# Kernel optimization log

Measured on AMD Instinct MI355X. Metric: run time of the kernel, lower is better.

The kernel has to match this reference:

```python
import jax, jax.numpy as jnp
import numpy as np
from jax import lax

NGTH = 15  # num_gth_mem
EPS = 1e-5  # BatchNorm eps


def _conv(x, w, b):
    y = lax.conv_general_dilated(x, w, (1, 1), 'VALID',
                                 dimension_numbers=('NCHW', 'OIHW', 'NCHW'))
    return y + b[None, :, None, None]


def _bn(x, g, b, m, v):
    # eval-mode BatchNorm2d with running stats
    return g[None, :, None, None] * (x - m[None, :, None, None]) * lax.rsqrt(v[None, :, None, None] + EPS) + b[None, :, None, None]


def _masked_stats(x, w):
    # x: (B, M, ...) ; w: (B, M) float weights. Population mean/std over masked mem slots.
    extra = (1,) * (x.ndim - 2)
    we = w.reshape(w.shape[:2] + extra)
    cnt = jnp.sum(w, axis=1).reshape((w.shape[0],) + extra)
    s = jnp.sum(x * we, axis=1)
    ss = jnp.sum(x * x * we, axis=1)
    mean = s / cnt
    var = jnp.maximum(ss / cnt - mean * mean, 0.0)
    return mean, jnp.sqrt(var)


def _forward(target_scores, ptm, pmt, predicted_iou, mem_mask, params):
    nf, ns, nmem, c, h, w = ptm.shape
    B = nf * ns
    ts = target_scores.reshape(B, 1, h, w)
    pmt = pmt.reshape(B, nmem, 1, h, w)
    ptm = ptm.reshape(B, nmem, c, h, w)
    mask = mem_mask.reshape(B, nmem)
    piou = predicted_iou.reshape(B, 1, 1, 1)

    mf = mask.astype(ts.dtype)
    # rank of each selected slot within the masked (ordered) selection
    rank = jnp.cumsum(mf, axis=1) - 1.0
    gth_w = mf * (rank < NGTH).astype(ts.dtype)   # first NGTH selected slots
    oth_w = mf * (rank >= NGTH).astype(ts.dtype)  # remaining selected slots

    max_ts = jnp.max(ts.reshape(B, -1), axis=1)

    pmt_mean, pmt_std = _masked_stats(pmt, mf)                 # (B,1,h,w)
    pmt_gth = pmt[:, :NGTH]                                    # unmasked slice (as in torch code)
    pmt_gth_mean = jnp.mean(pmt_gth, axis=1)
    pmt_gth_std = jnp.std(pmt_gth, axis=1)
    pmt_oth_mean, pmt_oth_std = _masked_stats(pmt, oth_w)

    ptm_max = jnp.max(ptm.reshape(B, nmem, -1), axis=2)        # (B, nmem)
    m_mm, s_mm = _masked_stats(ptm_max, mf)
    m_gm, s_gm = _masked_stats(ptm_max, gth_w)
    m_om, s_om = _masked_stats(ptm_max, oth_w)

    def bcast(v):
        return jnp.broadcast_to(v.reshape(B, 1, 1, 1), (B, 1, h, w))

    inp = jnp.concatenate([
        bcast(max_ts), jnp.broadcast_to(piou, (B, 1, h, w)),
        pmt_mean, pmt_std, pmt_gth_mean, pmt_gth_std, pmt_oth_mean, pmt_oth_std,
        bcast(m_mm), bcast(s_mm), bcast(m_gm), bcast(s_gm), bcast(m_om), bcast(s_om)
    ], axis=1)  # (B, 14, h, w)

    (c1w, c1b, g1, b1, m1, v1, c2w, c2b, g2, b2, m2, v2,
     c3w, c3b, g3, b3, m3, v3, c4w, c4b) = params
    x = jax.nn.relu(_bn(_conv(inp, c1w, c1b), g1, b1, m1, v1))
    x = lax.reduce_window(x, -jnp.inf, lax.max, (1, 1, 2, 2), (1, 1, 2, 2), 'VALID')
    x = jax.nn.relu(_bn(_conv(x, c2w, c2b), g2, b2, m2, v2))
    x = jax.nn.relu(_bn(_conv(x, c3w, c3b), g3, b3, m3, v3))
    x = _conv(x, c4w, c4b)
    return jnp.max(x, axis=(2, 3), keepdims=True)  # AdaptiveMaxPool2d((1,1)) -> (B,1,1,1)


def setup_inputs() -> dict:
    key = jax.random.key(0)
    ks = jax.random.split(key, 16)
    nf, ns, nmem, h, w = 16, 32, 30, 32, 32
    d = {}
    d['target_scores'] = jax.random.normal(ks[0], (nf, ns, 1, h, w), jnp.float32)
    d['ptm'] = jax.random.uniform(ks[1], (nf, ns, nmem, 1, h, w), jnp.float32)
    d['pmt'] = jax.random.uniform(ks[2], (nf, ns, nmem, 1, h, w), jnp.float32)
    d['predicted_iou'] = jax.random.uniform(ks[3], (nf, ns), jnp.float32)
    mask = jax.random.uniform(ks[4], (nf, ns, nmem)) < 0.7
    mask = mask.at[..., :20].set(True)  # >= 20 selected -> 'other' set non-empty
    d['mem_mask'] = mask
    d['conv1_w'] = jax.random.normal(ks[5], (64, 14, 3, 3), jnp.float32) * 0.1
    d['conv1_b'] = jnp.zeros((64,), jnp.float32)
    d['bn1_g'] = jnp.ones((64,), jnp.float32); d['bn1_b'] = jnp.zeros((64,), jnp.float32)
    d['bn1_m'] = jnp.zeros((64,), jnp.float32); d['bn1_v'] = jnp.ones((64,), jnp.float32)
    d['conv2_w'] = jax.random.normal(ks[6], (64, 64, 3, 3), jnp.float32) * 0.05
    d['conv2_b'] = jnp.zeros((64,), jnp.float32)
    d['bn2_g'] = jnp.ones((64,), jnp.float32); d['bn2_b'] = jnp.zeros((64,), jnp.float32)
    d['bn2_m'] = jnp.zeros((64,), jnp.float32); d['bn2_v'] = jnp.ones((64,), jnp.float32)
    d['conv3_w'] = jax.random.normal(ks[7], (64, 64, 3, 3), jnp.float32) * 0.05
    d['conv3_b'] = jnp.zeros((64,), jnp.float32)
    d['bn3_g'] = jnp.ones((64,), jnp.float32); d['bn3_b'] = jnp.zeros((64,), jnp.float32)
    d['bn3_m'] = jnp.zeros((64,), jnp.float32); d['bn3_v'] = jnp.ones((64,), jnp.float32)
    d['conv4_w'] = jax.random.normal(ks[8], (1, 64, 3, 3), jnp.float32) * 0.05
    d['conv4_b'] = jnp.zeros((1,), jnp.float32)
    return d


def reference(target_scores, ptm, pmt, predicted_iou, mem_mask,
              conv1_w, conv1_b, bn1_g, bn1_b, bn1_m, bn1_v,
              conv2_w, conv2_b, bn2_g, bn2_b, bn2_m, bn2_v,
              conv3_w, conv3_b, bn3_g, bn3_b, bn3_m, bn3_v,
              conv4_w, conv4_b):
    params = (conv1_w, conv1_b, bn1_g, bn1_b, bn1_m, bn1_v,
              conv2_w, conv2_b, bn2_g, bn2_b, bn2_m, bn2_v,
              conv3_w, conv3_b, bn3_g, bn3_b, bn3_m, bn3_v,
              conv4_w, conv4_b)
    return _forward(target_scores, ptm, pmt, predicted_iou, mem_mask, params)
```

## Files before the change

### kernel.cpp

```cpp
#include <hip/hip_runtime.h>
#include <math.h>

#define NFB  512
#define NMEM 30
#define PIX  1024
#define EPSF 1e-5f

typedef _Float16 half8_t __attribute__((ext_vector_type(8)));
typedef _Float16 half4_t __attribute__((ext_vector_type(4)));
typedef float float4_t __attribute__((ext_vector_type(4)));

#define OFF_W2R   13631488
#define OFF_W3R   13705216
#define OFF_WR1   13778944
#define OFF_WSUM1 13791232

__global__ __launch_bounds__(256) void k_prep(
    const float* __restrict__ c1w, const float* __restrict__ c2w,
    const float* __restrict__ c3w, _Float16* __restrict__ w2rep,
    _Float16* __restrict__ w3rep, _Float16* __restrict__ wr1,
    float* __restrict__ wsum1)
{
  int i = blockIdx.x * 256 + threadIdx.x;
  if (i < 36864) {
    int kr = i / 12288, rem = i - kr * 12288;
    int oc = rem / 192, k = rem - oc * 192;
    int kc = k >> 6, ci = k & 63;
    w2rep[i] = (_Float16)c2w[((oc * 64 + ci) * 3 + kr) * 3 + kc];
  } else if (i < 73728) {
    int j = i - 36864;
    int kr = j / 12288, rem = j - kr * 12288;
    int oc = rem / 192, k = rem - oc * 192;
    int kc = k >> 6, ci = k & 63;
    w3rep[j] = (_Float16)c3w[((oc * 64 + ci) * 3 + kr) * 3 + kc];
  } else if (i < 79872) {
    int j = i - 73728;
    int kr = j / 2048, rem = j - kr * 2048;
    int oc = rem >> 5, k = rem & 31;
    int kc = k >> 3, ci = k & 7;
    _Float16 v = (_Float16)0.f;
    if (kc < 3 && ci < 6)
      v = (_Float16)c1w[((oc * 14 + (2 + ci)) * 3 + kr) * 3 + kc];
    wr1[j] = v;
  } else if (i < 80384) {
    int j = i - 79872;
    int oc = j >> 3, u = j & 7;
    const int uch[8] = {0, 1, 8, 9, 10, 11, 12, 13};
    const float* wp = c1w + (oc * 14 + uch[u]) * 9;
    float s = 0.f;
    #pragma unroll
    for (int k = 0; k < 9; ++k) s += wp[k];
    wsum1[j] = s;
  }
}

__global__ __launch_bounds__(256, 2) void k_mega(
    const float* __restrict__ ts, const float* __restrict__ ptm,
    const float* __restrict__ pmt, const float* __restrict__ piou,
    const int* __restrict__ mask,
    const _Float16* __restrict__ wr1, const float* __restrict__ wsum1,
    const float* __restrict__ c1b, const float* __restrict__ g1,
    const float* __restrict__ b1, const float* __restrict__ m1,
    const float* __restrict__ v1,
    const _Float16* __restrict__ w2rep,
    const float* __restrict__ c2b, const float* __restrict__ g2,
    const float* __restrict__ b2, const float* __restrict__ m2,
    const float* __restrict__ v2,
    const _Float16* __restrict__ w3rep,
    const float* __restrict__ c3b, const float* __restrict__ g3,
    const float* __restrict__ b3, const float* __restrict__ m3,
    const float* __restrict__ v3,
    const float* __restrict__ c4w, const float* __restrict__ c4b,
    float* __restrict__ out)
{
  __shared__ __align__(16) char s_buf[55296];
  __shared__ float s_wm[NMEM], s_wo[NMEM], s_pmax[NMEM];
  __shared__ float s_red[4], s_scal[12], s_cnt[4];
  __shared__ float s_w4[576];

  const int b = blockIdx.x, t = threadIdx.x;
  const int lane = t & 63, wave = t >> 6;
  const int n16 = lane & 15, q = lane >> 4;
  _Float16* const IMG = (_Float16*)s_buf;
  _Float16* const X1  = (_Float16*)(s_buf + 16448);
  _Float16* const X2S = (_Float16*)s_buf;
  _Float16* const X3  = (_Float16*)(s_buf + 29952);

  for (int i = t; i < 576; i += 256) {
    int ci = i / 9, k = i - ci * 9;
    s_w4[k * 64 + ci] = c4w[i];
  }
  if (t == 0) {
    float cum = 0.f, cm = 0.f, cg = 0.f, co = 0.f;
    for (int m = 0; m < NMEM; ++m) {
      float f  = (mask[b * NMEM + m] != 0) ? 1.f : 0.f;
      float gg = (cum < 15.f) ? f : 0.f;
      float oo = f - gg;
      cum += f;
      s_wm[m] = f; s_wo[m] = oo;
      cm += f; cg += gg; co += oo;
    }
    s_cnt[0] = cm; s_cnt[1] = cg; s_cnt[2] = co;
  }
  {
    float4 u[8][4];
    const float* pb = ptm + (size_t)b * NMEM * PIX + lane * 4;
    #pragma unroll
    for (int k = 0; k < 8; ++k) {
      int m = wave + 4 * k;
      if (m < NMEM) {
        const float* p = pb + (size_t)m * PIX;
        #pragma unroll
        for (int j = 0; j < 4; ++j) u[k][j] = *(const float4*)(p + j * 256);
      }
    }
    #pragma unroll
    for (int k = 0; k < 8; ++k) {
      int m = wave + 4 * k;
      if (m < NMEM) {
        float4 v0 = u[k][0], v1_ = u[k][1], v2_ = u[k][2], v3_ = u[k][3];
        float mx = fmaxf(fmaxf(fmaxf(v0.x, v0.y), fmaxf(v0.z, v0.w)),
                         fmaxf(fmaxf(v1_.x, v1_.y), fmaxf(v1_.z, v1_.w)));
        mx = fmaxf(mx, fmaxf(fmaxf(fmaxf(v2_.x, v2_.y), fmaxf(v2_.z, v2_.w)),
                             fmaxf(fmaxf(v3_.x, v3_.y), fmaxf(v3_.z, v3_.w))));
        #pragma unroll
        for (int off = 32; off > 0; off >>= 1)
          mx = fmaxf(mx, __shfl_down(mx, off, 64));
        if (lane == 0) s_pmax[m] = mx;
      }
    }
  }
  {
    float4 v = ((const float4*)(ts + (size_t)b * PIX))[t];
    float mx = fmaxf(fmaxf(v.x, v.y), fmaxf(v.z, v.w));
    #pragma unroll
    for (int off = 32; off > 0; off >>= 1)
      mx = fmaxf(mx, __shfl_down(mx, off, 64));
    if (lane == 0) s_red[wave] = mx;
  }
  __syncthreads();
  if (t == 0) {
    float maxts = fmaxf(fmaxf(s_red[0], s_red[1]), fmaxf(s_red[2], s_red[3]));
    float sm = 0, sm2 = 0, sg = 0, sg2 = 0, so = 0, so2 = 0;
    for (int m = 0; m < NMEM; ++m) {
      float x = s_pmax[m];
      float gg = s_wm[m] - s_wo[m];
      sm += s_wm[m] * x;  sm2 += s_wm[m] * x * x;
      sg += gg * x;       sg2 += gg * x * x;
      so += s_wo[m] * x;  so2 += s_wo[m] * x * x;
    }
    float cm = s_cnt[0], cg = s_cnt[1], co = s_cnt[2];
    float a = sm / cm, g = sg / cg, o = so / co;
    s_scal[0] = maxts; s_scal[1] = piou[b];
    s_scal[2] = a; s_scal[3] = sqrtf(fmaxf(sm2 / cm - a * a, 0.f));
    s_scal[4] = g; s_scal[5] = sqrtf(fmaxf(sg2 / cg - g * g, 0.f));
    s_scal[6] = o; s_scal[7] = sqrtf(fmaxf(so2 / co - o * o, 0.f));
  }
  {
    const float cm = s_cnt[0], co = s_cnt[2];
    const int p0 = t * 4;
    const float* pb = pmt + (size_t)b * NMEM * PIX + p0;
    float4 va[15], vb[15];
    #pragma unroll
    for (int j = 0; j < 15; ++j) va[j] = *(const float4*)(pb + (size_t)j * PIX);
    #pragma unroll
    for (int j = 0; j < 15; ++j) vb[j] = *(const float4*)(pb + (size_t)(15 + j) * PIX);
    float sA[4] = {0,0,0,0}, qA[4] = {0,0,0,0};
    float sG[4] = {0,0,0,0}, qG[4] = {0,0,0,0};
    float sO[4] = {0,0,0,0}, qO[4] = {0,0,0,0};
    #pragma unroll
    for (int j = 0; j < 15; ++j) {
      float wm = s_wm[j], wo = s_wo[j];
      float xv[4] = {va[j].x, va[j].y, va[j].z, va[j].w};
      #pragma unroll
      for (int k = 0; k < 4; ++k) {
        float x = xv[k];
        sA[k] = fmaf(wm, x, sA[k]); qA[k] = fmaf(wm * x, x, qA[k]);
        sO[k] = fmaf(wo, x, sO[k]); qO[k] = fmaf(wo * x, x, qO[k]);
        sG[k] += x; qG[k] = fmaf(x, x, qG[k]);
      }
    }
    #pragma unroll
    for (int j = 0; j < 15; ++j) {
      float wm = s_wm[15 + j], wo = s_wo[15 + j];
      float xv[4] = {vb[j].x, vb[j].y, vb[j].z, vb[j].w};
      #pragma unroll
      for (int k = 0; k < 4; ++k) {
        float x = xv[k];
        sA[k] = fmaf(wm, x, sA[k]); qA[k] = fmaf(wm * x, x, qA[k]);
        sO[k] = fmaf(wo, x, sO[k]); qO[k] = fmaf(wo * x, x, qO[k]);
      }
    }
    half8_t* ob = (half8_t*)(IMG) + p0;
    #pragma unroll
    for (int j = 0; j < 4; ++j) {
      float m0 = sA[j] / cm;   float d0 = sqrtf(fmaxf(qA[j] / cm - m0 * m0, 0.f));
      float m1_ = sG[j] / 15.f; float d1 = sqrtf(fmaxf(qG[j] / 15.f - m1_ * m1_, 0.f));
      float m2_ = sO[j] / co;   float d2 = sqrtf(fmaxf(qO[j] / co - m2_ * m2_, 0.f));
      half8_t v;
      v[0] = (_Float16)m0;  v[1] = (_Float16)d0;
      v[2] = (_Float16)m1_; v[3] = (_Float16)d1;
      v[4] = (_Float16)m2_; v[5] = (_Float16)d2;
      v[6] = (_Float16)0.f; v[7] = (_Float16)0.f;
      ob[j] = v;
    }
    if (t < 4) {
      half8_t z = {(_Float16)0.f,(_Float16)0.f,(_Float16)0.f,(_Float16)0.f,
                   (_Float16)0.f,(_Float16)0.f,(_Float16)0.f,(_Float16)0.f};
      ((half8_t*)IMG)[1024 + t] = z;
    }
  }
  __syncthreads();

  {
    const int ocA = wave * 16 + n16;
    half8_t af[3];
    #pragma unroll
    for (int kr = 0; kr < 3; ++kr)
      af[kr] = *(const half8_t*)(wr1 + (kr * 64 + ocA) * 32 + q * 8);
    const int oc0 = wave * 16 + q * 4;
    float scv[4], shv[4], cst[4];
    #pragma unroll
    for (int rg = 0; rg < 4; ++rg) {
      int oc = oc0 + rg;
      float s = g1[oc] * rsqrtf(v1[oc] + EPSF);
      scv[rg] = s;
      shv[rg] = (c1b[oc] - m1[oc]) * s + b1[oc];
      float c = 0.f;
      #pragma unroll
      for (int u = 0; u < 8; ++u) c = fmaf(wsum1[oc * 8 + u], s_scal[u], c);
      cst[rg] = c;
    }
    #pragma unroll 1
    for (int pr = 0; pr < 15; ++pr) {
      const int r0 = pr * 2;
      float4_t acc[2][2];
      #pragma unroll
      for (int row = 0; row < 2; ++row)
        #pragma unroll
        for (int tt = 0; tt < 2; ++tt)
          acc[row][tt] = (float4_t){0.f, 0.f, 0.f, 0.f};
      #pragma unroll
      for (int row = 0; row < 2; ++row) {
        #pragma unroll
        for (int kr = 0; kr < 3; ++kr) {
          const int ip = (r0 + row + kr) * 32 + n16 + q;
          #pragma unroll
          for (int tt = 0; tt < 2; ++tt) {
            half8_t bf = *(const half8_t*)(IMG + (ip + tt * 16) * 8);
            acc[row][tt] = __builtin_amdgcn_mfma_f32_16x16x32_f16(
                af[kr], bf, acc[row][tt], 0, 0, 0);
          }
        }
      }
      #pragma unroll
      for (int tt = 0; tt < 2; ++tt) {
        float mm[4];
        #pragma unroll
        for (int j = 0; j < 4; ++j) {
          float m = fmaxf(acc[0][tt][j], acc[1][tt][j]);
          mm[j] = fmaxf(m, __shfl_xor(m, 1, 64));
        }
        if ((n16 & 1) == 0) {
          int pc = tt * 8 + (n16 >> 1);
          half4_t vv;
          if (pc < 15) {
            #pragma unroll
            for (int rg = 0; rg < 4; ++rg)
              vv[rg] = (_Float16)fmaxf(scv[rg] * (mm[rg] + cst[rg]) + shv[rg], 0.f);
          } else {
            vv[0] = (_Float16)0.f; vv[1] = (_Float16)0.f;
            vv[2] = (_Float16)0.f; vv[3] = (_Float16)0.f;
          }
          *(half4_t*)(X1 + (pr * 16 + pc) * 72 + oc0) = vv;
        }
      }
    }
  }
  __syncthreads();

  {
    int base72[11];
    #pragma unroll
    for (int nt = 0; nt < 11; ++nt) {
      int p = nt * 16 + n16;
      int pe = (p < 169) ? p : 168;
      int r = pe / 13, c = pe - r * 13;
      base72[nt] = (r * 16 + c) * 72;
    }
    float4_t acc[11];
    #pragma unroll
    for (int nt = 0; nt < 11; ++nt) acc[nt] = (float4_t){0.f, 0.f, 0.f, 0.f};
    const int ocA = wave * 16 + n16;
    half8_t af[3][6];
    #pragma unroll
    for (int kr = 0; kr < 3; ++kr) {
      const half8_t* wp = (const half8_t*)(w2rep + (size_t)(kr * 64 + ocA) * 192 + q * 8);
      #pragma unroll
      for (int ks = 0; ks < 6; ++ks) af[kr][ks] = wp[ks * 4];
    }
    #pragma unroll 1
    for (int kr = 0; kr < 3; ++kr) {
      const int krbase = kr * (16 * 72);
      #pragma unroll
      for (int ks = 0; ks < 6; ++ks) {
        const int k0 = ks * 32 + q * 8;
        const int kadd = krbase + (k0 >> 6) * 72 + (k0 & 63);
        #pragma unroll
        for (int nt = 0; nt < 11; ++nt) {
          half8_t bf = *(const half8_t*)(X1 + base72[nt] + kadd);
          acc[nt] = __builtin_amdgcn_mfma_f32_16x16x32_f16(af[kr][ks], bf, acc[nt], 0, 0, 0);
        }
      }
    }
    const int ocb = wave * 16 + q * 4;
    float scv[4], shv[4];
    #pragma unroll
    for (int rg = 0; rg < 4; ++rg) {
      int o = ocb + rg;
      float s = g2[o] * rsqrtf(v2[o] + EPSF);
      scv[rg] = s;
      shv[rg] = (c2b[o] - m2[o]) * s + b2[o];
    }
    half4_t vout[11];
    #pragma unroll
    for (int nt = 0; nt < 11; ++nt) {
      #pragma unroll
      for (int rg = 0; rg < 4; ++rg)
        vout[nt][rg] = (_Float16)fmaxf(acc[nt][rg] * scv[rg] + shv[rg], 0.f);
    }
    __syncthreads();
    #pragma unroll
    for (int nt = 0; nt < 11; ++nt) {
      int p = nt * 16 + n16;
      if (p < 169) {
        int r = p / 13, c = p - r * 13;
        *(half4_t*)(X2S + (r * 16 + c) * 72 + ocb) = vout[nt];
      }
    }
  }
  __syncthreads();

  {
    int base72[8];
    #pragma unroll
    for (int nt = 0; nt < 8; ++nt) {
      int p = nt * 16 + n16;
      int pe = (p < 121) ? p : 120;
      int r = pe / 11, c = pe - r * 11;
      base72[nt] = (r * 16 + c) * 72;
    }
    float4_t acc[8];
    #pragma unroll
    for (int nt = 0; nt < 8; ++nt) acc[nt] = (float4_t){0.f, 0.f, 0.f, 0.f};
    const int ocA = wave * 16 + n16;
    half8_t af[3][6];
    #pragma unroll
    for (int kr = 0; kr < 3; ++kr) {
      const half8_t* wp = (const half8_t*)(w3rep + (size_t)(kr * 64 + ocA) * 192 + q * 8);
      #pragma unroll
      for (int ks = 0; ks < 6; ++ks) af[kr][ks] = wp[ks * 4];
    }
    #pragma unroll 1
    for (int kr = 0; kr < 3; ++kr) {
      const int krbase = kr * (16 * 72);
      #pragma unroll
      for (int ks = 0; ks < 6; ++ks) {
        const int k0 = ks * 32 + q * 8;
        const int kadd = krbase + (k0 >> 6) * 72 + (k0 & 63);
        #pragma unroll
        for (int nt = 0; nt < 8; ++nt) {
          half8_t bf = *(const half8_t*)(X2S + base72[nt] + kadd);
          acc[nt] = __builtin_amdgcn_mfma_f32_16x16x32_f16(af[kr][ks], bf, acc[nt], 0, 0, 0);
        }
      }
    }
    const int ocb = wave * 16 + q * 4;
    float scv[4], shv[4];
    #pragma unroll
    for (int rg = 0; rg < 4; ++rg) {
      int o = ocb + rg;
      float s = g3[o] * rsqrtf(v3[o] + EPSF);
      scv[rg] = s;
      shv[rg] = (c3b[o] - m3[o]) * s + b3[o];
    }
    #pragma unroll
    for (int nt = 0; nt < 8; ++nt) {
      int p = nt * 16 + n16;
      if (p < 121) {
        int r = p / 11, c = p - r * 11;
        half4_t vv;
        #pragma unroll
        for (int rg = 0; rg < 4; ++rg)
          vv[rg] = (_Float16)fmaxf(acc[nt][rg] * scv[rg] + shv[rg], 0.f);
        *(half4_t*)(X3 + (r * 16 + c) * 72 + ocb) = vv;
      }
    }
  }
  __syncthreads();

  {
    float val = -INFINITY;
    if (t < 81) {
      const int r = t / 9, c = t - (t / 9) * 9;
      float acc = 0.f;
      #pragma unroll
      for (int kr = 0; kr < 3; ++kr)
        #pragma unroll
        for (int kc = 0; kc < 3; ++kc) {
          const _Float16* ip = X3 + ((r + kr) * 16 + (c + kc)) * 72;
          const float* wk = s_w4 + (kr * 3 + kc) * 64;
          #pragma unroll
          for (int cig = 0; cig < 8; ++cig) {
            half8_t x = *(const half8_t*)(ip + cig * 8);
            #pragma unroll
            for (int j = 0; j < 8; ++j)
              acc = fmaf((float)x[j], wk[cig * 8 + j], acc);
          }
        }
      val = acc;
    }
    #pragma unroll
    for (int off = 32; off > 0; off >>= 1)
      val = fmaxf(val, __shfl_down(val, off, 64));
    if (lane == 0) s_red[wave] = val;
    __syncthreads();
    if (t == 0)
      out[b] = fmaxf(fmaxf(s_red[0], s_red[1]), fmaxf(s_red[2], s_red[3])) + c4b[0];
  }
}

extern "C" void kernel_launch(void* const* d_in, const int* in_sizes, int n_in,
                              void* d_out, int out_size, void* d_ws, size_t ws_size,
                              hipStream_t stream) {
  const float* ts   = (const float*)d_in[0];
  const float* ptm  = (const float*)d_in[1];
  const float* pmt  = (const float*)d_in[2];
  const float* piou = (const float*)d_in[3];
  const int*   mask = (const int*)d_in[4];
  const float* c1w = (const float*)d_in[5];
  const float* c1b = (const float*)d_in[6];
  const float* g1  = (const float*)d_in[7];
  const float* b1  = (const float*)d_in[8];
  const float* m1  = (const float*)d_in[9];
  const float* v1  = (const float*)d_in[10];
  const float* c2w = (const float*)d_in[11];
  const float* c2b = (const float*)d_in[12];
  const float* g2  = (const float*)d_in[13];
  const float* b2  = (const float*)d_in[14];
  const float* m2  = (const float*)d_in[15];
  const float* v2  = (const float*)d_in[16];
  const float* c3w = (const float*)d_in[17];
  const float* c3b = (const float*)d_in[18];
  const float* g3  = (const float*)d_in[19];
  const float* b3  = (const float*)d_in[20];
  const float* m3  = (const float*)d_in[21];
  const float* v3  = (const float*)d_in[22];
  const float* c4w = (const float*)d_in[23];
  const float* c4b = (const float*)d_in[24];

  char* ws = (char*)d_ws;
  _Float16*  w2rep = (_Float16*)(ws + OFF_W2R);
  _Float16*  w3rep = (_Float16*)(ws + OFF_W3R);
  _Float16*  wr1   = (_Float16*)(ws + OFF_WR1);
  float*     wsum1 = (float*)(ws + OFF_WSUM1);

  k_prep<<<314, 256, 0, stream>>>(c1w, c2w, c3w, w2rep, w3rep, wr1, wsum1);
  k_mega<<<NFB, 256, 0, stream>>>(
      ts, ptm, pmt, piou, mask,
      wr1, wsum1, c1b, g1, b1, m1, v1,
      w2rep, c2b, g2, b2, m2, v2,
      w3rep, c3b, g3, b3, m3, v3,
      c4w, c4b, (float*)d_out);
}
```

Measured before the change: 246.3 us.

## Chunk pmt/ptm loads and double-buffer conv weight fragments to cut register pressure

The pmt statistics loop now loads the 30 memory slots in chunks of six with software prefetch, instead of holding all thirty float4 values in registers. Mask weights come from bitmasks rather than shared-memory floats. The ptm max pass is split into two passes of four slots each. Conv2 and conv3 weight fragments are double-buffered per kernel row (two sets of six) instead of all eighteen preloaded, overlapping the next row's weight load with the current row's MFMAs. The aim is fewer VGPRs at two blocks per CU, at the cost of less memory-level parallelism per thread.

```diff
diff --git a/kernel.cpp b/kernel.cpp
--- a/kernel.cpp
+++ b/kernel.cpp
@@ -54,6 +54,22 @@
   }
 }
 
+#define PROC_CHUNK(CC, BASE, N)                                     \
+  _Pragma("unroll")                                                 \
+  for (int j = 0; j < (N); ++j) {                                   \
+    const int mj = (BASE) + j;                                      \
+    float wm = ((mwm >> mj) & 1u) ? 1.f : 0.f;                      \
+    float wo = ((mwo >> mj) & 1u) ? 1.f : 0.f;                      \
+    float xv[4] = {CC[j].x, CC[j].y, CC[j].z, CC[j].w};             \
+    _Pragma("unroll")                                               \
+    for (int k = 0; k < 4; ++k) {                                   \
+      float x = xv[k];                                              \
+      sA[k] = fmaf(wm, x, sA[k]); qA[k] = fmaf(wm * x, x, qA[k]);   \
+      sO[k] = fmaf(wo, x, sO[k]); qO[k] = fmaf(wo * x, x, qO[k]);   \
+      if (mj < 15) { sG[k] += x; qG[k] = fmaf(x, x, qG[k]); }       \
+    }                                                               \
+  }
+
 __global__ __launch_bounds__(256, 2) void k_mega(
     const float* __restrict__ ts, const float* __restrict__ ptm,
     const float* __restrict__ pmt, const float* __restrict__ piou,
@@ -76,6 +92,7 @@
   __shared__ __align__(16) char s_buf[55296];
   __shared__ float s_wm[NMEM], s_wo[NMEM], s_pmax[NMEM];
   __shared__ float s_red[4], s_scal[12], s_cnt[4];
+  __shared__ unsigned s_mbits[2];
   __shared__ float s_w4[576];
 
   const int b = blockIdx.x, t = threadIdx.x;
@@ -92,41 +109,48 @@
   }
   if (t == 0) {
     float cum = 0.f, cm = 0.f, cg = 0.f, co = 0.f;
+    unsigned bm = 0u, bo = 0u;
     for (int m = 0; m < NMEM; ++m) {
       float f  = (mask[b * NMEM + m] != 0) ? 1.f : 0.f;
       float gg = (cum < 15.f) ? f : 0.f;
       float oo = f - gg;
       cum += f;
       s_wm[m] = f; s_wo[m] = oo;
+      if (f > 0.5f)  bm |= (1u << m);
+      if (oo > 0.5f) bo |= (1u << m);
       cm += f; cg += gg; co += oo;
     }
     s_cnt[0] = cm; s_cnt[1] = cg; s_cnt[2] = co;
-  }
-  {
-    float4 u[8][4];
+    s_mbits[0] = bm; s_mbits[1] = bo;
+  }
+  {
     const float* pb = ptm + (size_t)b * NMEM * PIX + lane * 4;
     #pragma unroll
-    for (int k = 0; k < 8; ++k) {
-      int m = wave + 4 * k;
-      if (m < NMEM) {
-        const float* p = pb + (size_t)m * PIX;
-        #pragma unroll
-        for (int j = 0; j < 4; ++j) u[k][j] = *(const float4*)(p + j * 256);
-      }
-    }
-    #pragma unroll
-    for (int k = 0; k < 8; ++k) {
-      int m = wave + 4 * k;
-      if (m < NMEM) {
-        float4 v0 = u[k][0], v1_ = u[k][1], v2_ = u[k][2], v3_ = u[k][3];
-        float mx = fmaxf(fmaxf(fmaxf(v0.x, v0.y), fmaxf(v0.z, v0.w)),
-                         fmaxf(fmaxf(v1_.x, v1_.y), fmaxf(v1_.z, v1_.w)));
-        mx = fmaxf(mx, fmaxf(fmaxf(fmaxf(v2_.x, v2_.y), fmaxf(v2_.z, v2_.w)),
-                             fmaxf(fmaxf(v3_.x, v3_.y), fmaxf(v3_.z, v3_.w))));
-        #pragma unroll
-        for (int off = 32; off > 0; off >>= 1)
-          mx = fmaxf(mx, __shfl_down(mx, off, 64));
-        if (lane == 0) s_pmax[m] = mx;
+    for (int pass = 0; pass < 2; ++pass) {
+      float4 u[4][4];
+      #pragma unroll
+      for (int k = 0; k < 4; ++k) {
+        int m = wave + 4 * (pass * 4 + k);
+        if (m < NMEM) {
+          #pragma unroll
+          for (int j = 0; j < 4; ++j)
+            u[k][j] = *(const float4*)(pb + (size_t)m * PIX + j * 256);
+        }
+      }
+      #pragma unroll
+      for (int k = 0; k < 4; ++k) {
+        int m = wave + 4 * (pass * 4 + k);
+        if (m < NMEM) {
+          float4 v0 = u[k][0], v1_ = u[k][1], v2_ = u[k][2], v3_ = u[k][3];
+          float mx = fmaxf(fmaxf(fmaxf(v0.x, v0.y), fmaxf(v0.z, v0.w)),
+                           fmaxf(fmaxf(v1_.x, v1_.y), fmaxf(v1_.z, v1_.w)));
+          mx = fmaxf(mx, fmaxf(fmaxf(fmaxf(v2_.x, v2_.y), fmaxf(v2_.z, v2_.w)),
+                               fmaxf(fmaxf(v3_.x, v3_.y), fmaxf(v3_.z, v3_.w))));
+          #pragma unroll
+          for (int off = 32; off > 0; off >>= 1)
+            mx = fmaxf(mx, __shfl_down(mx, off, 64));
+          if (lane == 0) s_pmax[m] = mx;
+        }
       }
     }
   }
@@ -157,40 +181,29 @@
     s_scal[6] = o; s_scal[7] = sqrtf(fmaxf(so2 / co - o * o, 0.f));
   }
   {
+    const unsigned mwm = s_mbits[0], mwo = s_mbits[1];
     const float cm = s_cnt[0], co = s_cnt[2];
     const int p0 = t * 4;
     const float* pb = pmt + (size_t)b * NMEM * PIX + p0;
-    float4 va[15], vb[15];
-    #pragma unroll
-    for (int j = 0; j < 15; ++j) va[j] = *(const float4*)(pb + (size_t)j * PIX);
-    #pragma unroll
-    for (int j = 0; j < 15; ++j) vb[j] = *(const float4*)(pb + (size_t)(15 + j) * PIX);
     float sA[4] = {0,0,0,0}, qA[4] = {0,0,0,0};
     float sG[4] = {0,0,0,0}, qG[4] = {0,0,0,0};
     float sO[4] = {0,0,0,0}, qO[4] = {0,0,0,0};
-    #pragma unroll
-    for (int j = 0; j < 15; ++j) {
-      float wm = s_wm[j], wo = s_wo[j];
-      float xv[4] = {va[j].x, va[j].y, va[j].z, va[j].w};
-      #pragma unroll
-      for (int k = 0; k < 4; ++k) {
-        float x = xv[k];
-        sA[k] = fmaf(wm, x, sA[k]); qA[k] = fmaf(wm * x, x, qA[k]);
-        sO[k] = fmaf(wo, x, sO[k]); qO[k] = fmaf(wo * x, x, qO[k]);
-        sG[k] += x; qG[k] = fmaf(x, x, qG[k]);
-      }
-    }
-    #pragma unroll
-    for (int j = 0; j < 15; ++j) {
-      float wm = s_wm[15 + j], wo = s_wo[15 + j];
-      float xv[4] = {vb[j].x, vb[j].y, vb[j].z, vb[j].w};
-      #pragma unroll
-      for (int k = 0; k < 4; ++k) {
-        float x = xv[k];
-        sA[k] = fmaf(wm, x, sA[k]); qA[k] = fmaf(wm * x, x, qA[k]);
-        sO[k] = fmaf(wo, x, sO[k]); qO[k] = fmaf(wo * x, x, qO[k]);
-      }
-    }
+    float4 c0[6], c1[6], c2[6], c3[6], c4[6];
+    #pragma unroll
+    for (int j = 0; j < 6; ++j) c0[j] = *(const float4*)(pb + (size_t)j * PIX);
+    #pragma unroll
+    for (int j = 0; j < 6; ++j) c1[j] = *(const float4*)(pb + (size_t)(6 + j) * PIX);
+    PROC_CHUNK(c0, 0, 6)
+    #pragma unroll
+    for (int j = 0; j < 6; ++j) c2[j] = *(const float4*)(pb + (size_t)(12 + j) * PIX);
+    PROC_CHUNK(c1, 6, 6)
+    #pragma unroll
+    for (int j = 0; j < 6; ++j) c3[j] = *(const float4*)(pb + (size_t)(18 + j) * PIX);
+    PROC_CHUNK(c2, 12, 6)
+    #pragma unroll
+    for (int j = 0; j < 6; ++j) c4[j] = *(const float4*)(pb + (size_t)(24 + j) * PIX);
+    PROC_CHUNK(c3, 18, 6)
+    PROC_CHUNK(c4, 24, 6)
     half8_t* ob = (half8_t*)(IMG) + p0;
     #pragma unroll
     for (int j = 0; j < 4; ++j) {
@@ -292,15 +305,8 @@
     #pragma unroll
     for (int nt = 0; nt < 11; ++nt) acc[nt] = (float4_t){0.f, 0.f, 0.f, 0.f};
     const int ocA = wave * 16 + n16;
-    half8_t af[3][6];
-    #pragma unroll
-    for (int kr = 0; kr < 3; ++kr) {
-      const half8_t* wp = (const half8_t*)(w2rep + (size_t)(kr * 64 + ocA) * 192 + q * 8);
-      #pragma unroll
-      for (int ks = 0; ks < 6; ++ks) af[kr][ks] = wp[ks * 4];
-    }
-    #pragma unroll 1
-    for (int kr = 0; kr < 3; ++kr) {
+
+    auto mfma_kr = [&](const half8_t (&af)[6], int kr) {
       const int krbase = kr * (16 * 72);
       #pragma unroll
       for (int ks = 0; ks < 6; ++ks) {
@@ -309,10 +315,31 @@
         #pragma unroll
         for (int nt = 0; nt < 11; ++nt) {
           half8_t bf = *(const half8_t*)(X1 + base72[nt] + kadd);
-          acc[nt] = __builtin_amdgcn_mfma_f32_16x16x32_f16(af[kr][ks], bf, acc[nt], 0, 0, 0);
-        }
-      }
-    }
+          acc[nt] = __builtin_amdgcn_mfma_f32_16x16x32_f16(af[ks], bf, acc[nt], 0, 0, 0);
+        }
+      }
+    };
+
+    half8_t afA[6], afB[6];
+    {
+      const half8_t* wp = (const half8_t*)(w2rep + (size_t)(0 * 64 + ocA) * 192 + q * 8);
+      #pragma unroll
+      for (int ks = 0; ks < 6; ++ks) afA[ks] = wp[ks * 4];
+    }
+    {
+      const half8_t* wp = (const half8_t*)(w2rep + (size_t)(1 * 64 + ocA) * 192 + q * 8);
+      #pragma unroll
+      for (int ks = 0; ks < 6; ++ks) afB[ks] = wp[ks * 4];
+      mfma_kr(afA, 0);
+    }
+    {
+      const half8_t* wp = (const half8_t*)(w2rep + (size_t)(2 * 64 + ocA) * 192 + q * 8);
+      #pragma unroll
+      for (int ks = 0; ks < 6; ++ks) afA[ks] = wp[ks * 4];
+      mfma_kr(afB, 1);
+    }
+    mfma_kr(afA, 2);
+
     const int ocb = wave * 16 + q * 4;
     float scv[4], shv[4];
     #pragma unroll
@@ -354,15 +381,8 @@
     #pragma unroll
     for (int nt = 0; nt < 8; ++nt) acc[nt] = (float4_t){0.f, 0.f, 0.f, 0.f};
     const int ocA = wave * 16 + n16;
-    half8_t af[3][6];
-    #pragma unroll
-    for (int kr = 0; kr < 3; ++kr) {
-      const half8_t* wp = (const half8_t*)(w3rep + (size_t)(kr * 64 + ocA) * 192 + q * 8);
-      #pragma unroll
-      for (int ks = 0; ks < 6; ++ks) af[kr][ks] = wp[ks * 4];
-    }
-    #pragma unroll 1
-    for (int kr = 0; kr < 3; ++kr) {
+
+    auto mfma_kr3 = [&](const half8_t (&af)[6], int kr) {
       const int krbase = kr * (16 * 72);
       #pragma unroll
       for (int ks = 0; ks < 6; ++ks) {
@@ -371,10 +391,31 @@
         #pragma unroll
         for (int nt = 0; nt < 8; ++nt) {
           half8_t bf = *(const half8_t*)(X2S + base72[nt] + kadd);
-          acc[nt] = __builtin_amdgcn_mfma_f32_16x16x32_f16(af[kr][ks], bf, acc[nt], 0, 0, 0);
-        }
-      }
-    }
+          acc[nt] = __builtin_amdgcn_mfma_f32_16x16x32_f16(af[ks], bf, acc[nt], 0, 0, 0);
+        }
+      }
+    };
+
+    half8_t afA[6], afB[6];
+    {
+      const half8_t* wp = (const half8_t*)(w3rep + (size_t)(0 * 64 + ocA) * 192 + q * 8);
+      #pragma unroll
+      for (int ks = 0; ks < 6; ++ks) afA[ks] = wp[ks * 4];
+    }
+    {
+      const half8_t* wp = (const half8_t*)(w3rep + (size_t)(1 * 64 + ocA) * 192 + q * 8);
+      #pragma unroll
+      for (int ks = 0; ks < 6; ++ks) afB[ks] = wp[ks * 4];
+      mfma_kr3(afA, 0);
+    }
+    {
+      const half8_t* wp = (const half8_t*)(w3rep + (size_t)(2 * 64 + ocA) * 192 + q * 8);
+      #pragma unroll
+      for (int ks = 0; ks < 6; ++ks) afA[ks] = wp[ks * 4];
+      mfma_kr3(afB, 1);
+    }
+    mfma_kr3(afA, 2);
+
     const int ocb = wave * 16 + q * 4;
     float scv[4], shv[4];
     #pragma unroll
```

Measured after the change: 228.4 us. 1.08x faster.
